# Kernel optimization log

Hardware: AMD Instinct MI355X
Metric: run time of the kernel (lower is better)

Reference implementation:

```python
import jax, jax.numpy as jnp
import numpy as np

B, N, F = 32, 1024, 128
H = 256        # n_hidden and mlp_hidden widths
OUT = 3
BN_EPS = 1e-3  # keras BatchNormalization default epsilon


def setup_inputs() -> dict:
    key = jax.random.key(0)
    ks = jax.random.split(key, 16)
    x = jax.random.normal(ks[0], (B, N, F), dtype=jnp.float32)
    a = (jax.random.uniform(ks[1], (B, N, N)) < 0.02).astype(jnp.float32)
    eps = jnp.zeros((), dtype=jnp.float32)  # trainable GIN epsilon, init 0

    def dense_p(k, fi, fo):
        k1, k2 = jax.random.split(k)
        w = jax.random.normal(k1, (fi, fo), dtype=jnp.float32) * (1.0 / np.sqrt(fi))
        b = jnp.zeros((fo,), dtype=jnp.float32)
        return w, b

    def bn_p(k, f):
        k1, k2 = jax.random.split(k)
        g = 1.0 + 0.1 * jax.random.normal(k1, (f,), dtype=jnp.float32)
        be = 0.1 * jax.random.normal(k2, (f,), dtype=jnp.float32)
        m = 0.1 * jax.random.normal(jax.random.fold_in(k, 7), (f,), dtype=jnp.float32)
        v = jnp.ones((f,), dtype=jnp.float32)
        return g, be, m, v

    w1, b1 = dense_p(ks[2], F, H)
    g1, be1, m1, v1 = bn_p(ks[3], H)
    w2, b2 = dense_p(ks[4], H, H)
    g2, be2, m2, v2 = bn_p(ks[5], H)
    w3, b3 = dense_p(ks[6], H, H)   # final MLP dense -> n_hidden
    g3, be3, m3, v3 = bn_p(ks[7], H)
    wd, bd = dense_p(ks[8], H, OUT)
    return dict(x=x, a=a, eps=eps,
                w1=w1, b1=b1, g1=g1, be1=be1, m1=m1, v1=v1,
                w2=w2, b2=b2, g2=g2, be2=be2, m2=m2, v2=v2,
                w3=w3, b3=b3, g3=g3, be3=be3, m3=m3, v3=v3,
                wd=wd, bd=bd)


def _bn(h, g, be, m, v):
    # inference-mode batchnorm over last (feature) axis
    return (h - m) * (g / jnp.sqrt(v + BN_EPS)) + be


def reference(x, a, eps, w1, b1, g1, be1, m1, v1,
              w2, b2, g2, be2, m2, v2,
              w3, b3, g3, be3, m3, v3, wd, bd):
    # GIN aggregation: (1+eps)*x_i + sum_{j in N(i)} x_j
    agg = jnp.einsum('bij,bjf->bif', a, x)          # [B,N,F]
    h = (1.0 + eps) * x + agg
    # MLP: Dense->BN->relu x2 (mlp_hidden), then Dense(n_hidden)->BN->relu
    h = jax.nn.relu(_bn(h @ w1 + b1, g1, be1, m1, v1))  # [B,N,H]
    h = jax.nn.relu(_bn(h @ w2 + b2, g2, be2, m2, v2))
    h = jax.nn.relu(_bn(h @ w3 + b3, g3, be3, m3, v3))
    # global max pool over nodes, dropout(0) = identity, then head Dense(3)
    pooled = jnp.max(h, axis=1)                      # [B,H]
    return pooled @ wd + bd                          # [B,3]
```

## Files before the change

kernel.cpp:

```cpp
#include <hip/hip_runtime.h>

#define BN_EPS 1e-3f

typedef __attribute__((ext_vector_type(8))) short bf16x8;
typedef __attribute__((ext_vector_type(4))) short short4v;
typedef __attribute__((ext_vector_type(4))) float f32x4;

__device__ __forceinline__ short f2bf(float f) {
    union { float f; unsigned u; } a; a.f = f;
    unsigned r = a.u + 0x7fffu + ((a.u >> 16) & 1u);
    return (short)(r >> 16);
}
__device__ __forceinline__ float bf2f(short s) {
    union { unsigned u; float f; } a;
    a.u = ((unsigned)(unsigned short)s) << 16;
    return a.f;
}

__global__ __launch_bounds__(512) void prep_x(const float* __restrict__ x,
                                              ushort* __restrict__ Xp) {
    const int b  = blockIdx.x >> 5;
    const int kc = blockIdx.x & 31;
    const int t  = threadIdx.x;
    const int f  = t & 127;
    const int kg = t >> 7;
    bf16x8 hi8, lo8;
    #pragma unroll
    for (int e = 0; e < 8; ++e) {
        const float val = x[((size_t)b * 1024 + kc * 32 + kg * 8 + e) * 128 + f];
        const short h = f2bf(val);
        hi8[e] = h; lo8[e] = f2bf(val - bf2f(h));
    }
    const size_t base = ((size_t)(b * 32 + kc)) * 8192 + (size_t)kg * 1024 + (size_t)f * 8;
    *reinterpret_cast<bf16x8*>(&Xp[base])        = hi8;
    *reinterpret_cast<bf16x8*>(&Xp[base + 4096]) = lo8;
}

__global__ __launch_bounds__(512, 4) void agg_mfma(
    const float* __restrict__ x, const float* __restrict__ a,
    const ushort* __restrict__ Xp, const float* __restrict__ epsp,
    float* __restrict__ h0) {
    __shared__ __align__(16) ushort Aab[4][64][8];
    __shared__ __align__(16) ushort Xhl[2][4][128][8];

    const int tid  = threadIdx.x;
    const int lane = tid & 63;
    const int wid  = tid >> 6;
    const int wr   = wid >> 1;
    const int wn   = wid & 1;
    const int lr   = lane & 15;
    const int kg   = lane >> 4;
    const int b    = blockIdx.x >> 4;
    const int row0 = (blockIdx.x & 15) * 64;

    const float*  ab = a + ((size_t)b * 1024 + row0) * 1024;
    const ushort* xp = Xp + (size_t)b * 32 * 8192;

    const int ai  = tid >> 3;
    const int akq = tid & 7;

    f32x4 acc[4] = {};

    for (int kc = 0; kc < 32; ++kc) {
        f32x4 av = *reinterpret_cast<const f32x4*>(ab + (size_t)ai * 1024 + kc * 32 + akq * 4);
        const f32x4* xsrc = reinterpret_cast<const f32x4*>(xp + (size_t)kc * 8192);
        f32x4 xv0 = xsrc[tid];
        f32x4 xv1 = xsrc[512 + tid];
        __syncthreads();
        {
            short4v h4;
            h4[0] = f2bf(av.x); h4[1] = f2bf(av.y);
            h4[2] = f2bf(av.z); h4[3] = f2bf(av.w);
            *reinterpret_cast<short4v*>(&Aab[akq >> 1][ai][(akq & 1) * 4]) = h4;
        }
        f32x4* xdst = reinterpret_cast<f32x4*>(Xhl);
        xdst[tid] = xv0; xdst[512 + tid] = xv1;
        __syncthreads();

        bf16x8 af = *reinterpret_cast<bf16x8*>(&Aab[kg][wr * 16 + lr][0]);
        #pragma unroll
        for (int ni = 0; ni < 4; ++ni) {
            bf16x8 bh = *reinterpret_cast<bf16x8*>(&Xhl[0][kg][wn * 64 + ni * 16 + lr][0]);
            bf16x8 bl = *reinterpret_cast<bf16x8*>(&Xhl[1][kg][wn * 64 + ni * 16 + lr][0]);
            acc[ni] = __builtin_amdgcn_mfma_f32_16x16x32_bf16(af, bh, acc[ni], 0, 0, 0);
            acc[ni] = __builtin_amdgcn_mfma_f32_16x16x32_bf16(af, bl, acc[ni], 0, 0, 0);
        }
    }

    const float ep1 = 1.0f + epsp[0];
    const float* xb = x + (size_t)b * 131072;
    #pragma unroll
    for (int ni = 0; ni < 4; ++ni) {
        const int col   = wn * 64 + ni * 16 + lr;
        const int rbase = row0 + wr * 16 + kg * 4;
        #pragma unroll
        for (int r = 0; r < 4; ++r) {
            const size_t off = (size_t)(rbase + r) * 128 + col;
            h0[(size_t)b * 131072 + off] = fmaf(ep1, xb[off], acc[ni][r]);
        }
    }
}

__global__ __launch_bounds__(256) void prep_w(
    const float* __restrict__ w1, const float* __restrict__ w2,
    const float* __restrict__ w3, ushort* __restrict__ Wp) {
    const int k = blockIdx.x;
    const int c = threadIdx.x;
    const float* src; int kl, base;
    if (k < 128)      { src = w1; kl = k;       base = 0; }
    else if (k < 384) { src = w2; kl = k - 128; base = 65536; }
    else              { src = w3; kl = k - 384; base = 196608; }
    const float val = src[(size_t)kl * 256 + c];
    const short hi = f2bf(val);
    const short lo = f2bf(val - bf2f(hi));
    const int off = base + (kl >> 5) * 16384 + ((((kl >> 3) & 3) * 256 + c) * 8) + (kl & 7);
    Wp[off]        = (ushort)hi;
    Wp[off + 8192] = (ushort)lo;
}

__global__ __launch_bounds__(512, 4) void fused_mlp(
    const float* __restrict__ h0, const ushort* __restrict__ Wp,
    const float* __restrict__ b1, const float* __restrict__ g1,
    const float* __restrict__ be1, const float* __restrict__ m1,
    const float* __restrict__ v1,
    const float* __restrict__ b2, const float* __restrict__ g2,
    const float* __restrict__ be2, const float* __restrict__ m2,
    const float* __restrict__ v2,
    const float* __restrict__ b3, const float* __restrict__ g3,
    const float* __restrict__ be3, const float* __restrict__ m3,
    const float* __restrict__ v3,
    float* __restrict__ pool) {
    __shared__ __align__(16) ushort Wb[2][4][256][8];
    __shared__ __align__(16) ushort Ab[2][2][4][32][8];

    const int tid  = threadIdx.x;
    const int lane = tid & 63;
    const int wid  = tid >> 6;
    const int wr   = wid >> 2;
    const int wn   = wid & 3;
    const int lr   = lane & 15;
    const int kg   = lane >> 4;
    const int row0 = blockIdx.x * 64;

    f32x4 acc1[2][4] = {};
    f32x4 acc2[2][4] = {};

    const int arow = tid >> 3;
    const int akq  = tid & 7;
    const float* aptr = h0 + (size_t)(row0 + arow) * 128 + akq * 4;

    #pragma unroll
    for (int kc = 0; kc < 4; ++kc) {
        f32x4 av = *reinterpret_cast<const f32x4*>(aptr + kc * 32);
        const f32x4* wsrc = reinterpret_cast<const f32x4*>(Wp + kc * 16384);
        f32x4 wv0 = wsrc[tid], wv1 = wsrc[512 + tid];
        f32x4 wv2 = wsrc[1024 + tid], wv3 = wsrc[1536 + tid];
        __syncthreads();
        {
            float fx[4] = {av.x, av.y, av.z, av.w};
            short4v h4, l4;
            #pragma unroll
            for (int e = 0; e < 4; ++e) {
                const short h = f2bf(fx[e]);
                h4[e] = h; l4[e] = f2bf(fx[e] - bf2f(h));
            }
            *reinterpret_cast<short4v*>(&Ab[0][arow >> 5][akq >> 1][arow & 31][(akq & 1) * 4]) = h4;
            *reinterpret_cast<short4v*>(&Ab[1][arow >> 5][akq >> 1][arow & 31][(akq & 1) * 4]) = l4;
        }
        f32x4* wdst = reinterpret_cast<f32x4*>(Wb);
        wdst[tid] = wv0; wdst[512 + tid] = wv1;
        wdst[1024 + tid] = wv2; wdst[1536 + tid] = wv3;
        __syncthreads();

        bf16x8 ah0 = *reinterpret_cast<bf16x8*>(&Ab[0][wr][kg][lr][0]);
        bf16x8 al0 = *reinterpret_cast<bf16x8*>(&Ab[1][wr][kg][lr][0]);
        bf16x8 ah1 = *reinterpret_cast<bf16x8*>(&Ab[0][wr][kg][16 + lr][0]);
        bf16x8 al1 = *reinterpret_cast<bf16x8*>(&Ab[1][wr][kg][16 + lr][0]);
        #pragma unroll
        for (int ni = 0; ni < 4; ++ni) {
            bf16x8 bh = *reinterpret_cast<bf16x8*>(&Wb[0][kg][wn * 64 + ni * 16 + lr][0]);
            bf16x8 bl = *reinterpret_cast<bf16x8*>(&Wb[1][kg][wn * 64 + ni * 16 + lr][0]);
            acc1[0][ni] = __builtin_amdgcn_mfma_f32_16x16x32_bf16(ah0, bh, acc1[0][ni], 0, 0, 0);
            acc1[0][ni] = __builtin_amdgcn_mfma_f32_16x16x32_bf16(ah0, bl, acc1[0][ni], 0, 0, 0);
            acc1[0][ni] = __builtin_amdgcn_mfma_f32_16x16x32_bf16(al0, bh, acc1[0][ni], 0, 0, 0);
            acc1[1][ni] = __builtin_amdgcn_mfma_f32_16x16x32_bf16(ah1, bh, acc1[1][ni], 0, 0, 0);
            acc1[1][ni] = __builtin_amdgcn_mfma_f32_16x16x32_bf16(ah1, bl, acc1[1][ni], 0, 0, 0);
            acc1[1][ni] = __builtin_amdgcn_mfma_f32_16x16x32_bf16(al1, bh, acc1[1][ni], 0, 0, 0);
        }
    }

    #pragma unroll
    for (int ni = 0; ni < 4; ++ni) {
        const int c = wn * 64 + ni * 16 + lr;
        const float s  = g1[c] * rsqrtf(v1[c] + BN_EPS);
        const float tt = be1[c] - m1[c] * s;
        const float bb = b1[c];
        #pragma unroll
        for (int mi = 0; mi < 2; ++mi)
            #pragma unroll
            for (int r = 0; r < 4; ++r)
                acc1[mi][ni][r] = fmaxf(fmaf(acc1[mi][ni][r] + bb, s, tt), 0.f);
    }

    #pragma unroll
    for (int kc = 0; kc < 8; ++kc) {
        const f32x4* wsrc = reinterpret_cast<const f32x4*>(Wp + 65536 + kc * 16384);
        f32x4 wv0 = wsrc[tid], wv1 = wsrc[512 + tid];
        f32x4 wv2 = wsrc[1024 + tid], wv3 = wsrc[1536 + tid];
        __syncthreads();
        if (wn == (kc >> 1)) {
            #pragma unroll
            for (int j = 0; j < 2; ++j) {
                const int ni  = (kc & 1) * 2 + j;
                const int kgw = j * 2 + (lr >> 3);
                const int e   = lr & 7;
                #pragma unroll
                for (int mi = 0; mi < 2; ++mi)
                    #pragma unroll
                    for (int r = 0; r < 4; ++r) {
                        const float val = acc1[mi][ni][r];
                        const short h = f2bf(val);
                        Ab[0][wr][kgw][mi * 16 + kg * 4 + r][e] = (ushort)h;
                        Ab[1][wr][kgw][mi * 16 + kg * 4 + r][e] = (ushort)f2bf(val - bf2f(h));
                    }
            }
        }
        f32x4* wdst = reinterpret_cast<f32x4*>(Wb);
        wdst[tid] = wv0; wdst[512 + tid] = wv1;
        wdst[1024 + tid] = wv2; wdst[1536 + tid] = wv3;
        __syncthreads();

        bf16x8 ah0 = *reinterpret_cast<bf16x8*>(&Ab[0][wr][kg][lr][0]);
        bf16x8 al0 = *reinterpret_cast<bf16x8*>(&Ab[1][wr][kg][lr][0]);
        bf16x8 ah1 = *reinterpret_cast<bf16x8*>(&Ab[0][wr][kg][16 + lr][0]);
        bf16x8 al1 = *reinterpret_cast<bf16x8*>(&Ab[1][wr][kg][16 + lr][0]);
        #pragma unroll
        for (int ni = 0; ni < 4; ++ni) {
            bf16x8 bh = *reinterpret_cast<bf16x8*>(&Wb[0][kg][wn * 64 + ni * 16 + lr][0]);
            bf16x8 bl = *reinterpret_cast<bf16x8*>(&Wb[1][kg][wn * 64 + ni * 16 + lr][0]);
            acc2[0][ni] = __builtin_amdgcn_mfma_f32_16x16x32_bf16(ah0, bh, acc2[0][ni], 0, 0, 0);
            acc2[0][ni] = __builtin_amdgcn_mfma_f32_16x16x32_bf16(ah0, bl, acc2[0][ni], 0, 0, 0);
            acc2[0][ni] = __builtin_amdgcn_mfma_f32_16x16x32_bf16(al0, bh, acc2[0][ni], 0, 0, 0);
            acc2[1][ni] = __builtin_amdgcn_mfma_f32_16x16x32_bf16(ah1, bh, acc2[1][ni], 0, 0, 0);
            acc2[1][ni] = __builtin_amdgcn_mfma_f32_16x16x32_bf16(ah1, bl, acc2[1][ni], 0, 0, 0);
            acc2[1][ni] = __builtin_amdgcn_mfma_f32_16x16x32_bf16(al1, bh, acc2[1][ni], 0, 0, 0);
        }
    }

    #pragma unroll
    for (int ni = 0; ni < 4; ++ni) {
        const int c = wn * 64 + ni * 16 + lr;
        const float s  = g2[c] * rsqrtf(v2[c] + BN_EPS);
        const float tt = be2[c] - m2[c] * s;
        const float bb = b2[c];
        #pragma unroll
        for (int mi = 0; mi < 2; ++mi)
            #pragma unroll
            for (int r = 0; r < 4; ++r)
                acc2[mi][ni][r] = fmaxf(fmaf(acc2[mi][ni][r] + bb, s, tt), 0.f);
    }

    #pragma unroll
    for (int mi = 0; mi < 2; ++mi)
        #pragma unroll
        for (int ni = 0; ni < 4; ++ni)
            #pragma unroll
            for (int r = 0; r < 4; ++r)
                acc1[mi][ni][r] = 0.f;

    #pragma unroll
    for (int kc = 0; kc < 8; ++kc) {
        const f32x4* wsrc = reinterpret_cast<const f32x4*>(Wp + 196608 + kc * 16384);
        f32x4 wv0 = wsrc[tid], wv1 = wsrc[512 + tid];
        f32x4 wv2 = wsrc[1024 + tid], wv3 = wsrc[1536 + tid];
        __syncthreads();
        if (wn == (kc >> 1)) {
            #pragma unroll
            for (int j = 0; j < 2; ++j) {
                const int ni  = (kc & 1) * 2 + j;
                const int kgw = j * 2 + (lr >> 3);
                const int e   = lr & 7;
                #pragma unroll
                for (int mi = 0; mi < 2; ++mi)
                    #pragma unroll
                    for (int r = 0; r < 4; ++r) {
                        const float val = acc2[mi][ni][r];
                        const short h = f2bf(val);
                        Ab[0][wr][kgw][mi * 16 + kg * 4 + r][e] = (ushort)h;
                        Ab[1][wr][kgw][mi * 16 + kg * 4 + r][e] = (ushort)f2bf(val - bf2f(h));
                    }
            }
        }
        f32x4* wdst = reinterpret_cast<f32x4*>(Wb);
        wdst[tid] = wv0; wdst[512 + tid] = wv1;
        wdst[1024 + tid] = wv2; wdst[1536 + tid] = wv3;
        __syncthreads();

        bf16x8 ah0 = *reinterpret_cast<bf16x8*>(&Ab[0][wr][kg][lr][0]);
        bf16x8 al0 = *reinterpret_cast<bf16x8*>(&Ab[1][wr][kg][lr][0]);
        bf16x8 ah1 = *reinterpret_cast<bf16x8*>(&Ab[0][wr][kg][16 + lr][0]);
        bf16x8 al1 = *reinterpret_cast<bf16x8*>(&Ab[1][wr][kg][16 + lr][0]);
        #pragma unroll
        for (int ni = 0; ni < 4; ++ni) {
            bf16x8 bh = *reinterpret_cast<bf16x8*>(&Wb[0][kg][wn * 64 + ni * 16 + lr][0]);
            bf16x8 bl = *reinterpret_cast<bf16x8*>(&Wb[1][kg][wn * 64 + ni * 16 + lr][0]);
            acc1[0][ni] = __builtin_amdgcn_mfma_f32_16x16x32_bf16(ah0, bh, acc1[0][ni], 0, 0, 0);
            acc1[0][ni] = __builtin_amdgcn_mfma_f32_16x16x32_bf16(ah0, bl, acc1[0][ni], 0, 0, 0);
            acc1[0][ni] = __builtin_amdgcn_mfma_f32_16x16x32_bf16(al0, bh, acc1[0][ni], 0, 0, 0);
            acc1[1][ni] = __builtin_amdgcn_mfma_f32_16x16x32_bf16(ah1, bh, acc1[1][ni], 0, 0, 0);
            acc1[1][ni] = __builtin_amdgcn_mfma_f32_16x16x32_bf16(ah1, bl, acc1[1][ni], 0, 0, 0);
            acc1[1][ni] = __builtin_amdgcn_mfma_f32_16x16x32_bf16(al1, bh, acc1[1][ni], 0, 0, 0);
        }
    }

    const int b = blockIdx.x >> 4;
    #pragma unroll
    for (int ni = 0; ni < 4; ++ni) {
        const int c = wn * 64 + ni * 16 + lr;
        const float s  = g3[c] * rsqrtf(v3[c] + BN_EPS);
        const float tt = be3[c] - m3[c] * s;
        const float bb = b3[c];
        float mx = 0.0f;
        #pragma unroll
        for (int mi = 0; mi < 2; ++mi)
            #pragma unroll
            for (int r = 0; r < 4; ++r)
                mx = fmaxf(mx, fmaf(acc1[mi][ni][r] + bb, s, tt));
        mx = fmaxf(mx, __shfl_xor(mx, 16));
        mx = fmaxf(mx, __shfl_xor(mx, 32));
        if (lane < 16)
            atomicMax((int*)&pool[b * 256 + c], __float_as_int(mx));
    }
}

__global__ __launch_bounds__(256) void pool_init(float* __restrict__ pool) {
    pool[blockIdx.x * 256 + threadIdx.x] = 0.0f;
}

__global__ __launch_bounds__(256) void head_kernel(const float* __restrict__ pool,
                                                   const float* __restrict__ wd,
                                                   const float* __restrict__ bd,
                                                   float* __restrict__ out) {
    const int b = blockIdx.x;
    const int t = threadIdx.x;
    const int w = t >> 6;
    const int lane = t & 63;
    if (w < 3) {
        float s = 0.f;
        #pragma unroll
        for (int k = 0; k < 256; k += 64)
            s += pool[b * 256 + k + lane] * wd[(k + lane) * 3 + w];
        #pragma unroll
        for (int off = 32; off; off >>= 1) s += __shfl_down(s, off);
        if (lane == 0) out[b * 3 + w] = s + bd[w];
    }
}

extern "C" void kernel_launch(void* const* d_in, const int* in_sizes, int n_in,
                              void* d_out, int out_size, void* d_ws, size_t ws_size,
                              hipStream_t stream) {
    const float* x   = (const float*)d_in[0];
    const float* a   = (const float*)d_in[1];
    const float* eps = (const float*)d_in[2];
    const float* w1  = (const float*)d_in[3];
    const float* b1  = (const float*)d_in[4];
    const float* g1  = (const float*)d_in[5];
    const float* be1 = (const float*)d_in[6];
    const float* m1  = (const float*)d_in[7];
    const float* v1  = (const float*)d_in[8];
    const float* w2  = (const float*)d_in[9];
    const float* b2  = (const float*)d_in[10];
    const float* g2  = (const float*)d_in[11];
    const float* be2 = (const float*)d_in[12];
    const float* m2  = (const float*)d_in[13];
    const float* v2  = (const float*)d_in[14];
    const float* w3  = (const float*)d_in[15];
    const float* b3  = (const float*)d_in[16];
    const float* g3  = (const float*)d_in[17];
    const float* be3 = (const float*)d_in[18];
    const float* m3  = (const float*)d_in[19];
    const float* v3  = (const float*)d_in[20];
    const float* wd  = (const float*)d_in[21];
    const float* bd  = (const float*)d_in[22];
    float* out = (float*)d_out;

    char* ws = (char*)d_ws;
    float*  h0   = (float*)(ws);
    ushort* Wp   = (ushort*)(ws + (16u << 20));
    ushort* Xp   = (ushort*)(ws + (18u << 20));
    float*  pool = (float*)(ws + (34u << 20));

    pool_init<<<32, 256, 0, stream>>>(pool);
    prep_w<<<640, 256, 0, stream>>>(w1, w2, w3, Wp);
    prep_x<<<1024, 512, 0, stream>>>(x, Xp);
    agg_mfma<<<512, 512, 0, stream>>>(x, a, Xp, eps, h0);
    fused_mlp<<<512, 512, 0, stream>>>(h0, Wp,
        b1, g1, be1, m1, v1,
        b2, g2, be2, m2, v2,
        b3, g3, be3, m3, v3, pool);
    head_kernel<<<32, 256, 0, stream>>>(pool, wd, bd, out);
}
```

Baseline: 316.0 us.

## Double-buffer LDS tiles in aggregation and fused MLP kernels with one barrier per step

Both the aggregation kernel and the fused MLP kernel now double-buffer their shared-memory tiles. The next chunk's global loads are issued before the current chunk's MFMAs, and the loaded data is written to the alternate buffer afterwards, so each step needs only one barrier instead of two. The aggregation kernel also processes two 32-wide K chunks per step, halving its iteration count. The aim is to hide global-load latency behind compute and cut barrier stalls. In exchange, LDS use doubles (the MLP kernel reaches about 64KB), which may lower occupancy below the requested 4 blocks per CU and adds register pressure.

```diff
diff --git a/kernel.cpp b/kernel.cpp
--- a/kernel.cpp
+++ b/kernel.cpp
@@ -40,8 +40,8 @@
     const float* __restrict__ x, const float* __restrict__ a,
     const ushort* __restrict__ Xp, const float* __restrict__ epsp,
     float* __restrict__ h0) {
-    __shared__ __align__(16) ushort Aab[4][64][8];
-    __shared__ __align__(16) ushort Xhl[2][4][128][8];
+    __shared__ __align__(16) ushort Aab[2][2][4][64][8];
+    __shared__ __align__(16) ushort Xhl[2][2][2][4][128][8];
 
     const int tid  = threadIdx.x;
     const int lane = tid & 63;
@@ -56,35 +56,56 @@
     const float*  ab = a + ((size_t)b * 1024 + row0) * 1024;
     const ushort* xp = Xp + (size_t)b * 32 * 8192;
 
-    const int ai  = tid >> 3;
+    const int ar  = tid >> 3;
     const int akq = tid & 7;
 
     f32x4 acc[4] = {};
 
-    for (int kc = 0; kc < 32; ++kc) {
-        f32x4 av = *reinterpret_cast<const f32x4*>(ab + (size_t)ai * 1024 + kc * 32 + akq * 4);
-        const f32x4* xsrc = reinterpret_cast<const f32x4*>(xp + (size_t)kc * 8192);
-        f32x4 xv0 = xsrc[tid];
-        f32x4 xv1 = xsrc[512 + tid];
+#define AGG_LOAD(S, AV0, AV1, XV0, XV1, XV2, XV3)                                         \
+    {   const float* ap_ = ab + (size_t)ar * 1024 + (S) * 64 + akq * 4;                   \
+        AV0 = *reinterpret_cast<const f32x4*>(ap_);                                       \
+        AV1 = *reinterpret_cast<const f32x4*>(ap_ + 32);                                  \
+        const f32x4* x0_ = reinterpret_cast<const f32x4*>(xp + (size_t)((S)*2    ) * 8192);\
+        const f32x4* x1_ = reinterpret_cast<const f32x4*>(xp + (size_t)((S)*2 + 1) * 8192);\
+        XV0 = x0_[tid]; XV1 = x0_[512 + tid]; XV2 = x1_[tid]; XV3 = x1_[512 + tid]; }
+
+#define AGG_WRITE(BUF, AV0, AV1, XV0, XV1, XV2, XV3)                                      \
+    {   float f0_[4] = {AV0.x, AV0.y, AV0.z, AV0.w};                                      \
+        float f1_[4] = {AV1.x, AV1.y, AV1.z, AV1.w};                                      \
+        short4v h0_, h1_;                                                                 \
+        _Pragma("unroll")                                                                 \
+        for (int e = 0; e < 4; ++e) { h0_[e] = f2bf(f0_[e]); h1_[e] = f2bf(f1_[e]); }     \
+        *reinterpret_cast<short4v*>(&Aab[BUF][0][akq >> 1][ar][(akq & 1) * 4]) = h0_;     \
+        *reinterpret_cast<short4v*>(&Aab[BUF][1][akq >> 1][ar][(akq & 1) * 4]) = h1_;     \
+        f32x4* xd_ = reinterpret_cast<f32x4*>(&Xhl[BUF][0][0][0][0][0]);                  \
+        xd_[tid] = XV0; xd_[512 + tid] = XV1; xd_[1024 + tid] = XV2; xd_[1536 + tid] = XV3; }
+
+    f32x4 av0, av1, xv0, xv1, xv2, xv3;
+    AGG_LOAD(0, av0, av1, xv0, xv1, xv2, xv3);
+    AGG_WRITE(0, av0, av1, xv0, xv1, xv2, xv3);
+
+    for (int s = 0; s < 16; ++s) {
+        const int buf = s & 1;
         __syncthreads();
-        {
-            short4v h4;
-            h4[0] = f2bf(av.x); h4[1] = f2bf(av.y);
-            h4[2] = f2bf(av.z); h4[3] = f2bf(av.w);
-            *reinterpret_cast<short4v*>(&Aab[akq >> 1][ai][(akq & 1) * 4]) = h4;
+        f32x4 nav0, nav1, nxv0, nxv1, nxv2, nxv3;
+        if (s + 1 < 16) AGG_LOAD(s + 1, nav0, nav1, nxv0, nxv1, nxv2, nxv3);
+
+        bf16x8 af0 = *reinterpret_cast<bf16x8*>(&Aab[buf][0][kg][wr * 16 + lr][0]);
+        bf16x8 af1 = *reinterpret_cast<bf16x8*>(&Aab[buf][1][kg][wr * 16 + lr][0]);
+        #pragma unroll
+        for (int ni = 0; ni < 4; ++ni) {
+            const int c = wn * 64 + ni * 16 + lr;
+            bf16x8 bh0 = *reinterpret_cast<bf16x8*>(&Xhl[buf][0][0][kg][c][0]);
+            bf16x8 bl0 = *reinterpret_cast<bf16x8*>(&Xhl[buf][0][1][kg][c][0]);
+            bf16x8 bh1 = *reinterpret_cast<bf16x8*>(&Xhl[buf][1][0][kg][c][0]);
+            bf16x8 bl1 = *reinterpret_cast<bf16x8*>(&Xhl[buf][1][1][kg][c][0]);
+            acc[ni] = __builtin_amdgcn_mfma_f32_16x16x32_bf16(af0, bh0, acc[ni], 0, 0, 0);
+            acc[ni] = __builtin_amdgcn_mfma_f32_16x16x32_bf16(af0, bl0, acc[ni], 0, 0, 0);
+            acc[ni] = __builtin_amdgcn_mfma_f32_16x16x32_bf16(af1, bh1, acc[ni], 0, 0, 0);
+            acc[ni] = __builtin_amdgcn_mfma_f32_16x16x32_bf16(af1, bl1, acc[ni], 0, 0, 0);
         }
-        f32x4* xdst = reinterpret_cast<f32x4*>(Xhl);
-        xdst[tid] = xv0; xdst[512 + tid] = xv1;
-        __syncthreads();
-
-        bf16x8 af = *reinterpret_cast<bf16x8*>(&Aab[kg][wr * 16 + lr][0]);
-        #pragma unroll
-        for (int ni = 0; ni < 4; ++ni) {
-            bf16x8 bh = *reinterpret_cast<bf16x8*>(&Xhl[0][kg][wn * 64 + ni * 16 + lr][0]);
-            bf16x8 bl = *reinterpret_cast<bf16x8*>(&Xhl[1][kg][wn * 64 + ni * 16 + lr][0]);
-            acc[ni] = __builtin_amdgcn_mfma_f32_16x16x32_bf16(af, bh, acc[ni], 0, 0, 0);
-            acc[ni] = __builtin_amdgcn_mfma_f32_16x16x32_bf16(af, bl, acc[ni], 0, 0, 0);
-        }
+
+        if (s + 1 < 16) AGG_WRITE(buf ^ 1, nav0, nav1, nxv0, nxv1, nxv2, nxv3);
     }
 
     const float ep1 = 1.0f + epsp[0];
@@ -99,6 +120,8 @@
             h0[(size_t)b * 131072 + off] = fmaf(ep1, xb[off], acc[ni][r]);
         }
     }
+#undef AGG_LOAD
+#undef AGG_WRITE
 }
 
 __global__ __launch_bounds__(256) void prep_w(
@@ -130,8 +153,8 @@
     const float* __restrict__ be3, const float* __restrict__ m3,
     const float* __restrict__ v3,
     float* __restrict__ pool) {
-    __shared__ __align__(16) ushort Wb[2][4][256][8];
-    __shared__ __align__(16) ushort Ab[2][2][4][32][8];
+    __shared__ __align__(16) ushort Wb[2][2][4][256][8];
+    __shared__ __align__(16) ushort Ab[2][2][2][4][32][8];
 
     const int tid  = threadIdx.x;
     const int lane = tid & 63;
@@ -142,123 +165,116 @@
     const int kg   = lane >> 4;
     const int row0 = blockIdx.x * 64;
 
+    const int ar  = tid >> 3;
+    const int akq = tid & 7;
+
     f32x4 acc1[2][4] = {};
     f32x4 acc2[2][4] = {};
 
-    const int arow = tid >> 3;
-    const int akq  = tid & 7;
-    const float* aptr = h0 + (size_t)(row0 + arow) * 128 + akq * 4;
-
-    #pragma unroll
-    for (int kc = 0; kc < 4; ++kc) {
-        f32x4 av = *reinterpret_cast<const f32x4*>(aptr + kc * 32);
-        const f32x4* wsrc = reinterpret_cast<const f32x4*>(Wp + kc * 16384);
-        f32x4 wv0 = wsrc[tid], wv1 = wsrc[512 + tid];
-        f32x4 wv2 = wsrc[1024 + tid], wv3 = wsrc[1536 + tid];
+#define MLP_LOADW(BASE, KC, W0, W1, W2, W3)                                               \
+    {   const f32x4* ws_ = reinterpret_cast<const f32x4*>(Wp + (BASE) + (KC) * 16384);    \
+        W0 = ws_[tid]; W1 = ws_[512 + tid]; W2 = ws_[1024 + tid]; W3 = ws_[1536 + tid]; }
+
+#define MLP_WRITEW(BUF, W0, W1, W2, W3)                                                   \
+    {   f32x4* wd_ = reinterpret_cast<f32x4*>(&Wb[BUF][0][0][0][0]);                      \
+        wd_[tid] = W0; wd_[512 + tid] = W1; wd_[1024 + tid] = W2; wd_[1536 + tid] = W3; }
+
+#define MLP_LOADA1(KC, AV)                                                                \
+    AV = *reinterpret_cast<const f32x4*>(h0 + (size_t)(row0 + ar) * 128 + (KC) * 32 + akq * 4);
+
+#define MLP_WRITEA1(BUF, AV)                                                              \
+    {   float fx_[4] = {AV.x, AV.y, AV.z, AV.w};                                          \
+        short4v h4_, l4_;                                                                 \
+        _Pragma("unroll")                                                                 \
+        for (int e = 0; e < 4; ++e) {                                                     \
+            const short h_ = f2bf(fx_[e]);                                                \
+            h4_[e] = h_; l4_[e] = f2bf(fx_[e] - bf2f(h_));                                \
+        }                                                                                 \
+        *reinterpret_cast<short4v*>(&Ab[BUF][0][ar >> 5][akq >> 1][ar & 31][(akq & 1) * 4]) = h4_; \
+        *reinterpret_cast<short4v*>(&Ab[BUF][1][ar >> 5][akq >> 1][ar & 31][(akq & 1) * 4]) = l4_; }
+
+#define MLP_REDIST(BUF, KC, SRC)                                                          \
+    if (wn == ((KC) >> 1)) {                                                              \
+        _Pragma("unroll")                                                                 \
+        for (int j = 0; j < 2; ++j) {                                                     \
+            const int ni  = ((KC) & 1) * 2 + j;                                           \
+            const int kgw = j * 2 + (lr >> 3);                                            \
+            const int e   = lr & 7;                                                       \
+            _Pragma("unroll")                                                             \
+            for (int mi = 0; mi < 2; ++mi)                                                \
+                _Pragma("unroll")                                                         \
+                for (int r = 0; r < 4; ++r) {                                             \
+                    const float val_ = SRC[mi][ni][r];                                    \
+                    const short h_ = f2bf(val_);                                          \
+                    Ab[BUF][0][wr][kgw][mi * 16 + kg * 4 + r][e] = (ushort)h_;            \
+                    Ab[BUF][1][wr][kgw][mi * 16 + kg * 4 + r][e] = (ushort)f2bf(val_ - bf2f(h_)); \
+                }                                                                         \
+        }                                                                                 \
+    }
+
+#define MLP_COMPUTE(BUF, DST)                                                             \
+    {   bf16x8 ah0 = *reinterpret_cast<bf16x8*>(&Ab[BUF][0][wr][kg][lr][0]);              \
+        bf16x8 al0 = *reinterpret_cast<bf16x8*>(&Ab[BUF][1][wr][kg][lr][0]);              \
+        bf16x8 ah1 = *reinterpret_cast<bf16x8*>(&Ab[BUF][0][wr][kg][16 + lr][0]);         \
+        bf16x8 al1 = *reinterpret_cast<bf16x8*>(&Ab[BUF][1][wr][kg][16 + lr][0]);         \
+        _Pragma("unroll")                                                                 \
+        for (int ni = 0; ni < 4; ++ni) {                                                  \
+            bf16x8 bh = *reinterpret_cast<bf16x8*>(&Wb[BUF][0][kg][wn * 64 + ni * 16 + lr][0]); \
+            bf16x8 bl = *reinterpret_cast<bf16x8*>(&Wb[BUF][1][kg][wn * 64 + ni * 16 + lr][0]); \
+            DST[0][ni] = __builtin_amdgcn_mfma_f32_16x16x32_bf16(ah0, bh, DST[0][ni], 0, 0, 0); \
+            DST[0][ni] = __builtin_amdgcn_mfma_f32_16x16x32_bf16(ah0, bl, DST[0][ni], 0, 0, 0); \
+            DST[0][ni] = __builtin_amdgcn_mfma_f32_16x16x32_bf16(al0, bh, DST[0][ni], 0, 0, 0); \
+            DST[1][ni] = __builtin_amdgcn_mfma_f32_16x16x32_bf16(ah1, bh, DST[1][ni], 0, 0, 0); \
+            DST[1][ni] = __builtin_amdgcn_mfma_f32_16x16x32_bf16(ah1, bl, DST[1][ni], 0, 0, 0); \
+            DST[1][ni] = __builtin_amdgcn_mfma_f32_16x16x32_bf16(al1, bh, DST[1][ni], 0, 0, 0); \
+        }                                                                                 \
+    }
+
+#define MLP_BN(ACC, G, V, BE, M, BI)                                                      \
+    _Pragma("unroll")                                                                     \
+    for (int ni = 0; ni < 4; ++ni) {                                                      \
+        const int c = wn * 64 + ni * 16 + lr;                                             \
+        const float s_  = G[c] * rsqrtf(V[c] + BN_EPS);                                   \
+        const float tt_ = BE[c] - M[c] * s_;                                              \
+        const float bb_ = BI[c];                                                          \
+        _Pragma("unroll")                                                                 \
+        for (int mi = 0; mi < 2; ++mi)                                                    \
+            _Pragma("unroll")                                                             \
+            for (int r = 0; r < 4; ++r)                                                   \
+                ACC[mi][ni][r] = fmaxf(fmaf(ACC[mi][ni][r] + bb_, s_, tt_), 0.f);         \
+    }
+
+    f32x4 wv0, wv1, wv2, wv3, wn0, wn1, wn2, wn3, av, avn;
+
+    MLP_LOADW(0, 0, wv0, wv1, wv2, wv3);
+    MLP_LOADA1(0, av);
+    MLP_WRITEW(0, wv0, wv1, wv2, wv3);
+    MLP_WRITEA1(0, av);
+
+    #pragma unroll
+    for (int s = 0; s < 4; ++s) {
+        const int buf = s & 1;
         __syncthreads();
-        {
-            float fx[4] = {av.x, av.y, av.z, av.w};
-            short4v h4, l4;
-            #pragma unroll
-            for (int e = 0; e < 4; ++e) {
-                const short h = f2bf(fx[e]);
-                h4[e] = h; l4[e] = f2bf(fx[e] - bf2f(h));
-            }
-            *reinterpret_cast<short4v*>(&Ab[0][arow >> 5][akq >> 1][arow & 31][(akq & 1) * 4]) = h4;
-            *reinterpret_cast<short4v*>(&Ab[1][arow >> 5][akq >> 1][arow & 31][(akq & 1) * 4]) = l4;
-        }
-        f32x4* wdst = reinterpret_cast<f32x4*>(Wb);
-        wdst[tid] = wv0; wdst[512 + tid] = wv1;
-        wdst[1024 + tid] = wv2; wdst[1536 + tid] = wv3;
+        if (s < 3) { MLP_LOADW(0, s + 1, wn0, wn1, wn2, wn3); MLP_LOADA1(s + 1, avn); }
+        else       { MLP_LOADW(65536, 0, wn0, wn1, wn2, wn3); }
+        MLP_COMPUTE(buf, acc1);
+        MLP_WRITEW(buf ^ 1, wn0, wn1, wn2, wn3);
+        if (s < 3) MLP_WRITEA1(buf ^ 1, avn);
+    }
+    MLP_BN(acc1, g1, v1, be1, m1, b1);
+    MLP_REDIST(0, 0, acc1);
+
+    #pragma unroll
+    for (int s = 0; s < 8; ++s) {
+        const int buf = s & 1;
         __syncthreads();
-
-        bf16x8 ah0 = *reinterpret_cast<bf16x8*>(&Ab[0][wr][kg][lr][0]);
-        bf16x8 al0 = *reinterpret_cast<bf16x8*>(&Ab[1][wr][kg][lr][0]);
-        bf16x8 ah1 = *reinterpret_cast<bf16x8*>(&Ab[0][wr][kg][16 + lr][0]);
-        bf16x8 al1 = *reinterpret_cast<bf16x8*>(&Ab[1][wr][kg][16 + lr][0]);
-        #pragma unroll
-        for (int ni = 0; ni < 4; ++ni) {
-            bf16x8 bh = *reinterpret_cast<bf16x8*>(&Wb[0][kg][wn * 64 + ni * 16 + lr][0]);
-            bf16x8 bl = *reinterpret_cast<bf16x8*>(&Wb[1][kg][wn * 64 + ni * 16 + lr][0]);
-            acc1[0][ni] = __builtin_amdgcn_mfma_f32_16x16x32_bf16(ah0, bh, acc1[0][ni], 0, 0, 0);
-            acc1[0][ni] = __builtin_amdgcn_mfma_f32_16x16x32_bf16(ah0, bl, acc1[0][ni], 0, 0, 0);
-            acc1[0][ni] = __builtin_amdgcn_mfma_f32_16x16x32_bf16(al0, bh, acc1[0][ni], 0, 0, 0);
-            acc1[1][ni] = __builtin_amdgcn_mfma_f32_16x16x32_bf16(ah1, bh, acc1[1][ni], 0, 0, 0);
-            acc1[1][ni] = __builtin_amdgcn_mfma_f32_16x16x32_bf16(ah1, bl, acc1[1][ni], 0, 0, 0);
-            acc1[1][ni] = __builtin_amdgcn_mfma_f32_16x16x32_bf16(al1, bh, acc1[1][ni], 0, 0, 0);
-        }
-    }
-
-    #pragma unroll
-    for (int ni = 0; ni < 4; ++ni) {
-        const int c = wn * 64 + ni * 16 + lr;
-        const float s  = g1[c] * rsqrtf(v1[c] + BN_EPS);
-        const float tt = be1[c] - m1[c] * s;
-        const float bb = b1[c];
-        #pragma unroll
-        for (int mi = 0; mi < 2; ++mi)
-            #pragma unroll
-            for (int r = 0; r < 4; ++r)
-                acc1[mi][ni][r] = fmaxf(fmaf(acc1[mi][ni][r] + bb, s, tt), 0.f);
-    }
-
-    #pragma unroll
-    for (int kc = 0; kc < 8; ++kc) {
-        const f32x4* wsrc = reinterpret_cast<const f32x4*>(Wp + 65536 + kc * 16384);
-        f32x4 wv0 = wsrc[tid], wv1 = wsrc[512 + tid];
-        f32x4 wv2 = wsrc[1024 + tid], wv3 = wsrc[1536 + tid];
-        __syncthreads();
-        if (wn == (kc >> 1)) {
-            #pragma unroll
-            for (int j = 0; j < 2; ++j) {
-                const int ni  = (kc & 1) * 2 + j;
-                const int kgw = j * 2 + (lr >> 3);
-                const int e   = lr & 7;
-                #pragma unroll
-                for (int mi = 0; mi < 2; ++mi)
-                    #pragma unroll
-                    for (int r = 0; r < 4; ++r) {
-                        const float val = acc1[mi][ni][r];
-                        const short h = f2bf(val);
-                        Ab[0][wr][kgw][mi * 16 + kg * 4 + r][e] = (ushort)h;
-                        Ab[1][wr][kgw][mi * 16 + kg * 4 + r][e] = (ushort)f2bf(val - bf2f(h));
-                    }
-            }
-        }
-        f32x4* wdst = reinterpret_cast<f32x4*>(Wb);
-        wdst[tid] = wv0; wdst[512 + tid] = wv1;
-        wdst[1024 + tid] = wv2; wdst[1536 + tid] = wv3;
-        __syncthreads();
-
-        bf16x8 ah0 = *reinterpret_cast<bf16x8*>(&Ab[0][wr][kg][lr][0]);
-        bf16x8 al0 = *reinterpret_cast<bf16x8*>(&Ab[1][wr][kg][lr][0]);
-        bf16x8 ah1 = *reinterpret_cast<bf16x8*>(&Ab[0][wr][kg][16 + lr][0]);
-        bf16x8 al1 = *reinterpret_cast<bf16x8*>(&Ab[1][wr][kg][16 + lr][0]);
-        #pragma unroll
-        for (int ni = 0; ni < 4; ++ni) {
-            bf16x8 bh = *reinterpret_cast<bf16x8*>(&Wb[0][kg][wn * 64 + ni * 16 + lr][0]);
-            bf16x8 bl = *reinterpret_cast<bf16x8*>(&Wb[1][kg][wn * 64 + ni * 16 + lr][0]);
-            acc2[0][ni] = __builtin_amdgcn_mfma_f32_16x16x32_bf16(ah0, bh, acc2[0][ni], 0, 0, 0);
-            acc2[0][ni] = __builtin_amdgcn_mfma_f32_16x16x32_bf16(ah0, bl, acc2[0][ni], 0, 0, 0);
-            acc2[0][ni] = __builtin_amdgcn_mfma_f32_16x16x32_bf16(al0, bh, acc2[0][ni], 0, 0, 0);
-            acc2[1][ni] = __builtin_amdgcn_mfma_f32_16x16x32_bf16(ah1, bh, acc2[1][ni], 0, 0, 0);
-            acc2[1][ni] = __builtin_amdgcn_mfma_f32_16x16x32_bf16(ah1, bl, acc2[1][ni], 0, 0, 0);
-            acc2[1][ni] = __builtin_amdgcn_mfma_f32_16x16x32_bf16(al1, bh, acc2[1][ni], 0, 0, 0);
-        }
-    }
-
-    #pragma unroll
-    for (int ni = 0; ni < 4; ++ni) {
-        const int c = wn * 64 + ni * 16 + lr;
-        const float s  = g2[c] * rsqrtf(v2[c] + BN_EPS);
-        const float tt = be2[c] - m2[c] * s;
-        const float bb = b2[c];
-        #pragma unroll
-        for (int mi = 0; mi < 2; ++mi)
-            #pragma unroll
-            for (int r = 0; r < 4; ++r)
-                acc2[mi][ni][r] = fmaxf(fmaf(acc2[mi][ni][r] + bb, s, tt), 0.f);
-    }
+        if (s < 7) { MLP_LOADW(65536, s + 1, wn0, wn1, wn2, wn3); }
+        else       { MLP_LOADW(196608, 0, wn0, wn1, wn2, wn3); }
+        MLP_COMPUTE(buf, acc2);
+        MLP_WRITEW(buf ^ 1, wn0, wn1, wn2, wn3);
+        if (s < 7) MLP_REDIST(buf ^ 1, s + 1, acc1);
+    }
+    MLP_BN(acc2, g2, v2, be2, m2, b2);
 
     #pragma unroll
     for (int mi = 0; mi < 2; ++mi)
@@ -267,49 +283,17 @@
             #pragma unroll
             for (int r = 0; r < 4; ++r)
                 acc1[mi][ni][r] = 0.f;
-
-    #pragma unroll
-    for (int kc = 0; kc < 8; ++kc) {
-        const f32x4* wsrc = reinterpret_cast<const f32x4*>(Wp + 196608 + kc * 16384);
-        f32x4 wv0 = wsrc[tid], wv1 = wsrc[512 + tid];
-        f32x4 wv2 = wsrc[1024 + tid], wv3 = wsrc[1536 + tid];
+    MLP_REDIST(0, 0, acc2);
+
+    #pragma unroll
+    for (int s = 0; s < 8; ++s) {
+        const int buf = s & 1;
         __syncthreads();
-        if (wn == (kc >> 1)) {
-            #pragma unroll
-            for (int j = 0; j < 2; ++j) {
-                const int ni  = (kc & 1) * 2 + j;
-                const int kgw = j * 2 + (lr >> 3);
-                const int e   = lr & 7;
-                #pragma unroll
-                for (int mi = 0; mi < 2; ++mi)
-                    #pragma unroll
-                    for (int r = 0; r < 4; ++r) {
-                        const float val = acc2[mi][ni][r];
-                        const short h = f2bf(val);
-                        Ab[0][wr][kgw][mi * 16 + kg * 4 + r][e] = (ushort)h;
-                        Ab[1][wr][kgw][mi * 16 + kg * 4 + r][e] = (ushort)f2bf(val - bf2f(h));
-                    }
-            }
-        }
-        f32x4* wdst = reinterpret_cast<f32x4*>(Wb);
-        wdst[tid] = wv0; wdst[512 + tid] = wv1;
-        wdst[1024 + tid] = wv2; wdst[1536 + tid] = wv3;
-        __syncthreads();
-
-        bf16x8 ah0 = *reinterpret_cast<bf16x8*>(&Ab[0][wr][kg][lr][0]);
-        bf16x8 al0 = *reinterpret_cast<bf16x8*>(&Ab[1][wr][kg][lr][0]);
-        bf16x8 ah1 = *reinterpret_cast<bf16x8*>(&Ab[0][wr][kg][16 + lr][0]);
-        bf16x8 al1 = *reinterpret_cast<bf16x8*>(&Ab[1][wr][kg][16 + lr][0]);
-        #pragma unroll
-        for (int ni = 0; ni < 4; ++ni) {
-            bf16x8 bh = *reinterpret_cast<bf16x8*>(&Wb[0][kg][wn * 64 + ni * 16 + lr][0]);
-            bf16x8 bl = *reinterpret_cast<bf16x8*>(&Wb[1][kg][wn * 64 + ni * 16 + lr][0]);
-            acc1[0][ni] = __builtin_amdgcn_mfma_f32_16x16x32_bf16(ah0, bh, acc1[0][ni], 0, 0, 0);
-            acc1[0][ni] = __builtin_amdgcn_mfma_f32_16x16x32_bf16(ah0, bl, acc1[0][ni], 0, 0, 0);
-            acc1[0][ni] = __builtin_amdgcn_mfma_f32_16x16x32_bf16(al0, bh, acc1[0][ni], 0, 0, 0);
-            acc1[1][ni] = __builtin_amdgcn_mfma_f32_16x16x32_bf16(ah1, bh, acc1[1][ni], 0, 0, 0);
-            acc1[1][ni] = __builtin_amdgcn_mfma_f32_16x16x32_bf16(ah1, bl, acc1[1][ni], 0, 0, 0);
-            acc1[1][ni] = __builtin_amdgcn_mfma_f32_16x16x32_bf16(al1, bh, acc1[1][ni], 0, 0, 0);
+        if (s < 7) { MLP_LOADW(196608, s + 1, wn0, wn1, wn2, wn3); }
+        MLP_COMPUTE(buf, acc1);
+        if (s < 7) {
+            MLP_WRITEW(buf ^ 1, wn0, wn1, wn2, wn3);
+            MLP_REDIST(buf ^ 1, s + 1, acc2);
         }
     }
 
```

Measured after the change: 304.9 us. -3.5%, faster.
